# Kernel optimization log

Hardware: AMD Instinct MI355X
Metric: run time of the kernel (lower is better)

Reference implementation:

```python
import jax, jax.numpy as jnp
import numpy as np

B, H, S, D = 2, 12, 2048, 64

def setup_inputs() -> dict:
    key = jax.random.key(0)
    kq, kk, kv = jax.random.split(key, 3)
    Q = jax.random.normal(kq, (B, H, S, D), dtype=jnp.float32)
    K = jax.random.normal(kk, (B, H, S, D), dtype=jnp.float32)
    V = jax.random.normal(kv, (B, H, S, D), dtype=jnp.float32)
    return {"Q": Q, "K": K, "V": V}

def reference(Q, K, V):
    # NOTE: original code scales by sqrt(Q.shape[-2]) (the sequence length),
    # not the head dim — reproduced faithfully.
    scale = 1.0 / np.sqrt(Q.shape[-2]).astype(np.float32)
    scores = jnp.einsum('bhqd,bhkd->bhqk', Q, K) * scale  # [B,H,S,S]
    attn = jax.nn.softmax(scores, axis=-1)
    context = jnp.einsum('bhqk,bhkd->bhqd', attn, V)      # [B,H,S,D]
    # torch .squeeze(-1) only removes the last dim if it is size 1; D=64 so no-op
    return context
```

## Files before the change

kernel.cpp:

```cpp
#include <hip/hip_runtime.h>
#include <hip/hip_bf16.h>
#include <math.h>
#include <stdint.h>

#define BATCH 2
#define NH 12
#define SEQ 2048
#define HD 64
#define TQ 64
#define TK 64
#define NHEADS (BATCH*NH)
#define NIT (SEQ / TK)

typedef short bf16x8 __attribute__((ext_vector_type(8)));
typedef float f32x4 __attribute__((ext_vector_type(4)));
typedef float f32x16 __attribute__((ext_vector_type(16)));
typedef unsigned short us4_t __attribute__((ext_vector_type(4)));
typedef unsigned short us8_t __attribute__((ext_vector_type(8)));
typedef unsigned int u32x4 __attribute__((ext_vector_type(4)));

#if __has_builtin(__builtin_amdgcn_exp2f)
#define EXP2F(x) __builtin_amdgcn_exp2f(x)
#else
#define EXP2F(x) exp2f(x)
#endif

static __device__ __forceinline__ unsigned short f2bf(float f) {
    unsigned int u = __float_as_uint(f);
    u += 0x7fffu + ((u >> 16) & 1u);
    return (unsigned short)(u >> 16);
}

static __device__ __forceinline__ unsigned int pack2bf(float a, float b) {
    __hip_bfloat162 v = __float22bfloat162_rn(float2{a, b});
    return *(unsigned int*)&v;
}

static __device__ __forceinline__ void async_cp16(const void* g, void* l) {
    __builtin_amdgcn_global_load_lds(
        (const __attribute__((address_space(1))) void*)g,
        (__attribute__((address_space(3))) void*)(uintptr_t)l,
        16, 0, 0);
}

static __device__ __forceinline__ int tile_off(int r, int c) {
    int rp  = r >> 1;
    int pos = (((r & 1) << 3) | c) ^ (rp & 15);
    return rp * 128 + pos * 8;
}

__global__ __launch_bounds__(256)
void prep_kv(const float* __restrict__ K, const float* __restrict__ V,
             unsigned short* __restrict__ Kb, unsigned short* __restrict__ Vtb) {
    __shared__ unsigned short T[64][66];
    const int bh = blockIdx.x >> 5;
    const int s0 = (blockIdx.x & 31) * 64;
    const int tid = threadIdx.x;
    const size_t off = ((size_t)bh * SEQ + s0) * HD;

    #pragma unroll
    for (int u = 0; u < 4; ++u) {
        int idx = u * 1024 + tid * 4;
        float4 a = *(const float4*)&K[off + idx];
        us4_t r4 = { f2bf(a.x), f2bf(a.y), f2bf(a.z), f2bf(a.w) };
        *(us4_t*)&Kb[off + idx] = r4;
    }
    #pragma unroll
    for (int u = 0; u < 4; ++u) {
        int idx = u * 1024 + tid * 4;
        int r = idx >> 6, col = idx & 63;
        float4 a = *(const float4*)&V[off + idx];
        *(unsigned int*)&T[r][col]     = pack2bf(a.x, a.y);
        *(unsigned int*)&T[r][col + 2] = pack2bf(a.z, a.w);
    }
    __syncthreads();
    unsigned short* Vdst = Vtb + (size_t)bh * HD * SEQ;
    const int g = tid & 7, dd = tid >> 3;
    #pragma unroll
    for (int h = 0; h < 2; ++h) {
        int d = dd + 32 * h;
        us8_t r8;
        #pragma unroll
        for (int j = 0; j < 8; ++j) {
            int src = ((g >> 1) << 4) + ((j >> 2) << 3) + ((g & 1) << 2) + (j & 3);
            r8[j] = T[src][d];
        }
        *(us8_t*)&Vdst[(size_t)d * SEQ + s0 + g * 8] = r8;
    }
}

__global__ __launch_bounds__(256, 3)
void fa_main(const float* __restrict__ Q,
             const unsigned short* __restrict__ Kb,
             const unsigned short* __restrict__ Vtb,
             float* __restrict__ O, float qs) {
    const int x  = blockIdx.x & 7;
    const int t  = blockIdx.x >> 3;
    const int bh = x + 8 * (t % 3);
    const int qt = t / 3;
    const int q0 = qt * TQ;

    __shared__ __align__(16) unsigned char SH[33280];
    unsigned short* Ksh0 = (unsigned short*)SH;
    unsigned short* Ksh1 = (unsigned short*)(SH + 8192);
    unsigned short* Vsh0 = (unsigned short*)(SH + 16384);
    unsigned short* Vsh1 = (unsigned short*)(SH + 24576);
    float* Lsum = (float*)(SH + 32768);
    float* Linv = (float*)(SH + 33024);
    float* ORed = (float*)SH;

    const int tid  = threadIdx.x;
    const int w    = tid >> 6;
    const int mt   = w >> 1;
    const int nt   = w & 1;
    const int lane = tid & 63;
    const int l31  = lane & 31;
    const int hi   = lane >> 5;

    const float*          Qh = Q   + ((size_t)bh * SEQ + q0) * HD;
    const unsigned short* Kh = Kb  + (size_t)bh * SEQ * HD;
    const unsigned short* Vh = Vtb + (size_t)bh * HD * SEQ;

    int rS[2], cS[2];
    #pragma unroll
    for (int i = 0; i < 2; ++i) {
        int rp = w * 8 + 4 * i + (lane >> 4);
        int lc = (lane & 15) ^ (rp & 15);
        rS[i] = 2 * rp + (lc >> 3);
        cS[i] = lc & 7;
    }
    const int dst0 = (w * 8 + 0) * 128, dst1 = (w * 8 + 4) * 128;
    const size_t kG0 = (size_t)rS[0] * HD  + cS[0] * 8;
    const size_t kG1 = (size_t)rS[1] * HD  + cS[1] * 8;
    const size_t vG0 = (size_t)rS[0] * SEQ + cS[0] * 8;
    const size_t vG1 = (size_t)rS[1] * SEQ + cS[1] * 8;

    async_cp16(Kh + kG0, &Ksh0[dst0]);
    async_cp16(Kh + kG1, &Ksh0[dst1]);
    async_cp16(Vh + vG0, &Vsh0[dst0]);
    async_cp16(Vh + vG1, &Vsh0[dst1]);
    #pragma unroll
    for (int u = 0; u < 4; ++u) {
        int idx = u * 1024 + tid * 4;
        int r = idx >> 6, col = idx & 63;
        float4 a = *(const float4*)&Qh[idx];
        uint2 pk = { pack2bf(a.x * qs, a.y * qs), pack2bf(a.z * qs, a.w * qs) };
        *(uint2*)&Vsh1[tile_off(r, col >> 3) + (col & 7)] = pk;
    }
    __syncthreads();

    bf16x8 qf[4];
    #pragma unroll
    for (int s = 0; s < 4; ++s)
        qf[s] = *(const bf16x8*)&Vsh1[tile_off(mt * 32 + l31, s * 2 + hi)];
    __syncthreads();

    int kOffL[4], vOffL[2][2];
    #pragma unroll
    for (int s = 0; s < 4; ++s) kOffL[s] = tile_off(nt * 32 + l31, s * 2 + hi);
    #pragma unroll
    for (int dt = 0; dt < 2; ++dt)
        #pragma unroll
        for (int ks = 0; ks < 2; ++ks)
            vOffL[dt][ks] = tile_off(dt * 32 + l31, nt * 4 + ks * 2 + hi);

    f32x16 o[2];
    o[0] = (f32x16)(0.f);
    o[1] = (f32x16)(0.f);
    float lsum = 0.f;

    #pragma unroll 2
    for (int it = 0; it < NIT; ++it) {
        const int cur = it & 1;
        if (it + 1 < NIT) {
            const size_t kv = (size_t)(it + 1) * TK;
            unsigned short* Kn = cur ? Ksh0 : Ksh1;
            unsigned short* Vn = cur ? Vsh0 : Vsh1;
            async_cp16(Kh + kv * HD + kG0, &Kn[dst0]);
            async_cp16(Kh + kv * HD + kG1, &Kn[dst1]);
            async_cp16(Vh + kv + vG0,      &Vn[dst0]);
            async_cp16(Vh + kv + vG1,      &Vn[dst1]);
        }
        const unsigned short* Ks = cur ? Ksh1 : Ksh0;
        const unsigned short* Vs = cur ? Vsh1 : Vsh0;

        bf16x8 vf[2][2];
        #pragma unroll
        for (int dt = 0; dt < 2; ++dt)
            #pragma unroll
            for (int ks = 0; ks < 2; ++ks)
                vf[dt][ks] = *(const bf16x8*)&Vs[vOffL[dt][ks]];

        f32x16 sc = (f32x16)(0.f);
        __builtin_amdgcn_s_setprio(1);
        #pragma unroll
        for (int s = 0; s < 4; ++s) {
            bf16x8 kf = *(const bf16x8*)&Ks[kOffL[s]];
            sc = __builtin_amdgcn_mfma_f32_32x32x16_bf16(kf, qf[s], sc, 0, 0, 0);
        }
        __builtin_amdgcn_s_setprio(0);

        float e0[8], e1[8];
        #pragma unroll
        for (int r = 0; r < 8; ++r) e0[r] = EXP2F(sc[r]);
        union { u32x4 d; bf16x8 h; } pu0, pu1;
        pu0.d = (u32x4){ pack2bf(e0[0], e0[1]), pack2bf(e0[2], e0[3]),
                         pack2bf(e0[4], e0[5]), pack2bf(e0[6], e0[7]) };
        bf16x8 pf0 = pu0.h;
        __builtin_amdgcn_s_setprio(1);
        o[0] = __builtin_amdgcn_mfma_f32_32x32x16_bf16(pf0, vf[0][0], o[0], 0, 0, 0);
        o[1] = __builtin_amdgcn_mfma_f32_32x32x16_bf16(pf0, vf[1][0], o[1], 0, 0, 0);
        __builtin_amdgcn_s_setprio(0);

        #pragma unroll
        for (int r = 0; r < 8; ++r) e1[r] = EXP2F(sc[8 + r]);
        pu1.d = (u32x4){ pack2bf(e1[0], e1[1]), pack2bf(e1[2], e1[3]),
                         pack2bf(e1[4], e1[5]), pack2bf(e1[6], e1[7]) };
        bf16x8 pf1 = pu1.h;
        __builtin_amdgcn_s_setprio(1);
        o[0] = __builtin_amdgcn_mfma_f32_32x32x16_bf16(pf1, vf[0][1], o[0], 0, 0, 0);
        o[1] = __builtin_amdgcn_mfma_f32_32x32x16_bf16(pf1, vf[1][1], o[1], 0, 0, 0);
        __builtin_amdgcn_s_setprio(0);

        float t0 = ((e0[0] + e0[1]) + (e0[2] + e0[3]))
                 + ((e0[4] + e0[5]) + (e0[6] + e0[7]));
        float t1 = ((e1[0] + e1[1]) + (e1[2] + e1[3]))
                 + ((e1[4] + e1[5]) + (e1[6] + e1[7]));
        lsum += t0 + t1;

        __syncthreads();
    }

    lsum += __shfl_xor(lsum, 32, 64);

    if (nt == 1) {
        if (lane < 32) Lsum[mt * 32 + lane] = lsum;
        #pragma unroll
        for (int dt = 0; dt < 2; ++dt) {
            const int d = dt * 32 + l31;
            #pragma unroll
            for (int g = 0; g < 4; ++g) {
                const int m0 = mt * 32 + 8 * g + 4 * hi;
                const int ph = (m0 >> 2) ^ (d & 15);
                float4 v = { o[dt][4*g+0], o[dt][4*g+1], o[dt][4*g+2], o[dt][4*g+3] };
                *(float4*)&ORed[d * 64 + ph * 4] = v;
            }
        }
    }
    __syncthreads();

    if (nt == 0) {
        float ltot = lsum + Lsum[mt * 32 + l31];
        if (lane < 32) Linv[mt * 32 + lane] = 1.0f / ltot;
        float* Oh = O + ((size_t)bh * SEQ + q0) * HD;
        #pragma unroll
        for (int dt = 0; dt < 2; ++dt) {
            const int d = dt * 32 + l31;
            #pragma unroll
            for (int g = 0; g < 4; ++g) {
                const int m0 = mt * 32 + 8 * g + 4 * hi;
                const int ph = (m0 >> 2) ^ (d & 15);
                float4 part = *(const float4*)&ORed[d * 64 + ph * 4];
                float4 inv4 = *(const float4*)&Linv[m0];
                const float* pp = (const float*)&part;
                const float* ii = (const float*)&inv4;
                #pragma unroll
                for (int j = 0; j < 4; ++j)
                    Oh[(size_t)(m0 + j) * HD + d] = (o[dt][4*g+j] + pp[j]) * ii[j];
            }
        }
    }
}

#define PAD 8
#define LSTR (HD + PAD)

__global__ __launch_bounds__(256)
void fa_fwd_fb(const float* __restrict__ Q, const float* __restrict__ K,
               const float* __restrict__ V, float* __restrict__ O) {
    const int x  = blockIdx.x & 7;
    const int t  = blockIdx.x >> 3;
    const int bh = x + 8 * (t % 3);
    const int qt = t / 3;
    const int q0 = qt * TQ;
    const long base = (long)bh * SEQ * HD;

    __shared__ unsigned short Qs[TQ][LSTR];
    __shared__ unsigned short Ks2[64][LSTR];
    __shared__ unsigned short Vt[HD][64 + PAD];
    __shared__ unsigned short Ps2[4][16][LSTR];

    const int tid  = threadIdx.x;
    const int wave = tid >> 6;
    const int lane = tid & 63;
    const int col  = lane & 15;
    const int quad = lane >> 4;
    const int m0   = wave * 16;

    #pragma unroll
    for (int i = 0; i < 4; ++i) {
        int idx = tid + 256 * i;
        int row = idx >> 4;
        int c4  = (idx & 15) * 4;
        float4 v = *(const float4*)&Q[base + (long)(q0 + row) * HD + c4];
        ushort4 b = { f2bf(v.x), f2bf(v.y), f2bf(v.z), f2bf(v.w) };
        *(ushort4*)&Qs[row][c4] = b;
    }
    __syncthreads();

    bf16x8 aq0 = *(const bf16x8*)&Qs[m0 + col][quad * 8];
    bf16x8 aq1 = *(const bf16x8*)&Qs[m0 + col][32 + quad * 8];

    f32x4 o0 = {0.f,0.f,0.f,0.f}, o1 = o0, o2 = o0, o3 = o0;
    float l[4] = {0.f, 0.f, 0.f, 0.f};
    const float scale = 0.022097086912079608f;

    for (int kv0 = 0; kv0 < SEQ; kv0 += 64) {
        __syncthreads();
        #pragma unroll
        for (int i = 0; i < 4; ++i) {
            int idx = tid + 256 * i;
            int row = idx >> 4;
            int c4  = (idx & 15) * 4;
            float4 kv = *(const float4*)&K[base + (long)(kv0 + row) * HD + c4];
            ushort4 kb = { f2bf(kv.x), f2bf(kv.y), f2bf(kv.z), f2bf(kv.w) };
            *(ushort4*)&Ks2[row][c4] = kb;
            float4 vv = *(const float4*)&V[base + (long)(kv0 + row) * HD + c4];
            Vt[c4 + 0][row] = f2bf(vv.x);
            Vt[c4 + 1][row] = f2bf(vv.y);
            Vt[c4 + 2][row] = f2bf(vv.z);
            Vt[c4 + 3][row] = f2bf(vv.w);
        }
        __syncthreads();

        f32x4 sc[4];
        #pragma unroll
        for (int n = 0; n < 4; ++n) {
            bf16x8 b0 = *(const bf16x8*)&Ks2[n * 16 + col][quad * 8];
            bf16x8 b1 = *(const bf16x8*)&Ks2[n * 16 + col][32 + quad * 8];
            f32x4 acc = {0.f,0.f,0.f,0.f};
            acc = __builtin_amdgcn_mfma_f32_16x16x32_bf16(aq0, b0, acc, 0, 0, 0);
            acc = __builtin_amdgcn_mfma_f32_16x16x32_bf16(aq1, b1, acc, 0, 0, 0);
            sc[n] = acc;
        }

        float tsum[4] = {0.f, 0.f, 0.f, 0.f};
        #pragma unroll
        for (int n = 0; n < 4; ++n) {
            #pragma unroll
            for (int r = 0; r < 4; ++r) {
                float p = __expf(sc[n][r] * scale);
                tsum[r] += p;
                Ps2[wave][quad * 4 + r][n * 16 + col] = f2bf(p);
            }
        }
        #pragma unroll
        for (int off = 1; off < 16; off <<= 1) {
            #pragma unroll
            for (int r = 0; r < 4; ++r) tsum[r] += __shfl_xor(tsum[r], off, 64);
        }
        #pragma unroll
        for (int r = 0; r < 4; ++r) l[r] += tsum[r];

        bf16x8 ap0 = *(const bf16x8*)&Ps2[wave][col][quad * 8];
        bf16x8 ap1 = *(const bf16x8*)&Ps2[wave][col][32 + quad * 8];
        #pragma unroll
        for (int n = 0; n < 4; ++n) {
            bf16x8 b0 = *(const bf16x8*)&Vt[n * 16 + col][quad * 8];
            bf16x8 b1 = *(const bf16x8*)&Vt[n * 16 + col][32 + quad * 8];
            f32x4* op = (n == 0) ? &o0 : (n == 1) ? &o1 : (n == 2) ? &o2 : &o3;
            *op = __builtin_amdgcn_mfma_f32_16x16x32_bf16(ap0, b0, *op, 0, 0, 0);
            *op = __builtin_amdgcn_mfma_f32_16x16x32_bf16(ap1, b1, *op, 0, 0, 0);
        }
    }

    float inv[4];
    #pragma unroll
    for (int r = 0; r < 4; ++r) inv[r] = 1.0f / l[r];
    #pragma unroll
    for (int r = 0; r < 4; ++r) {
        long row = base + (long)(q0 + m0 + quad * 4 + r) * HD;
        O[row +  0 + col] = o0[r] * inv[r];
        O[row + 16 + col] = o1[r] * inv[r];
        O[row + 32 + col] = o2[r] * inv[r];
        O[row + 48 + col] = o3[r] * inv[r];
    }
}

extern "C" void kernel_launch(void* const* d_in, const int* in_sizes, int n_in,
                              void* d_out, int out_size, void* d_ws, size_t ws_size,
                              hipStream_t stream) {
    const float* Q = (const float*)d_in[0];
    const float* K = (const float*)d_in[1];
    const float* V = (const float*)d_in[2];
    float* O = (float*)d_out;

    const size_t tensorElems = (size_t)NHEADS * SEQ * HD;
    const size_t need = 2 * tensorElems * sizeof(unsigned short);

    if (ws_size >= need) {
        unsigned short* Kb  = (unsigned short*)d_ws;
        unsigned short* Vtb = Kb + tensorElems;
        const float qs = (float)(1.4426950408889634 / sqrt(2048.0));
        prep_kv<<<dim3(NHEADS * (SEQ / 64)), dim3(256), 0, stream>>>(K, V, Kb, Vtb);
        fa_main<<<dim3(NHEADS * (SEQ / TQ)), dim3(256), 0, stream>>>(Q, Kb, Vtb, O, qs);
    } else {
        fa_fwd_fb<<<dim3(NHEADS * (SEQ / TQ)), dim3(256), 0, stream>>>(Q, K, V, O);
    }
}
```

Measured before the change: 116.7 us.

## Triple-buffer K/V tiles with prefetch distance two and explicit vmcnt waits

Replaces the double-buffered K/V shared-memory pipeline with a three-stage ring buffer. The Q staging moves to its own region, and tiles are prefetched two iterations ahead. The end-of-loop __syncthreads is replaced by an s_waitcnt vmcnt plus s_barrier at the top of the loop, so up to two tiles of loads can be in flight while compute runs. Shared memory grows from about 33KB to about 49KB per block, which may lower occupancy under the 3-blocks-per-CU launch bound.

```diff
diff --git a/kernel.cpp b/kernel.cpp
--- a/kernel.cpp
+++ b/kernel.cpp
@@ -100,14 +100,11 @@
     const int qt = t / 3;
     const int q0 = qt * TQ;
 
-    __shared__ __align__(16) unsigned char SH[33280];
-    unsigned short* Ksh0 = (unsigned short*)SH;
-    unsigned short* Ksh1 = (unsigned short*)(SH + 8192);
-    unsigned short* Vsh0 = (unsigned short*)(SH + 16384);
-    unsigned short* Vsh1 = (unsigned short*)(SH + 24576);
-    float* Lsum = (float*)(SH + 32768);
-    float* Linv = (float*)(SH + 33024);
+    __shared__ __align__(16) unsigned char SH[49664];
+    float* Lsum = (float*)(SH + 49152);
+    float* Linv = (float*)(SH + 49408);
     float* ORed = (float*)SH;
+    unsigned short* QS = (unsigned short*)(SH + 32768);
 
     const int tid  = threadIdx.x;
     const int w    = tid >> 6;
@@ -135,25 +132,38 @@
     const size_t vG0 = (size_t)rS[0] * SEQ + cS[0] * 8;
     const size_t vG1 = (size_t)rS[1] * SEQ + cS[1] * 8;
 
-    async_cp16(Kh + kG0, &Ksh0[dst0]);
-    async_cp16(Kh + kG1, &Ksh0[dst1]);
-    async_cp16(Vh + vG0, &Vsh0[dst0]);
-    async_cp16(Vh + vG1, &Vsh0[dst1]);
+    {
+        unsigned short* K0 = (unsigned short*)(SH);
+        unsigned short* V0 = (unsigned short*)(SH + 8192);
+        async_cp16(Kh + kG0, &K0[dst0]);
+        async_cp16(Kh + kG1, &K0[dst1]);
+        async_cp16(Vh + vG0, &V0[dst0]);
+        async_cp16(Vh + vG1, &V0[dst1]);
+    }
     #pragma unroll
     for (int u = 0; u < 4; ++u) {
         int idx = u * 1024 + tid * 4;
         int r = idx >> 6, col = idx & 63;
         float4 a = *(const float4*)&Qh[idx];
         uint2 pk = { pack2bf(a.x * qs, a.y * qs), pack2bf(a.z * qs, a.w * qs) };
-        *(uint2*)&Vsh1[tile_off(r, col >> 3) + (col & 7)] = pk;
+        *(uint2*)&QS[tile_off(r, col >> 3) + (col & 7)] = pk;
     }
     __syncthreads();
 
     bf16x8 qf[4];
     #pragma unroll
     for (int s = 0; s < 4; ++s)
-        qf[s] = *(const bf16x8*)&Vsh1[tile_off(mt * 32 + l31, s * 2 + hi)];
+        qf[s] = *(const bf16x8*)&QS[tile_off(mt * 32 + l31, s * 2 + hi)];
     __syncthreads();
+
+    {
+        unsigned short* K1 = (unsigned short*)(SH + 16384);
+        unsigned short* V1 = (unsigned short*)(SH + 16384 + 8192);
+        async_cp16(Kh + (size_t)TK * HD + kG0, &K1[dst0]);
+        async_cp16(Kh + (size_t)TK * HD + kG1, &K1[dst1]);
+        async_cp16(Vh + (size_t)TK + vG0,      &V1[dst0]);
+        async_cp16(Vh + (size_t)TK + vG1,      &V1[dst1]);
+    }
 
     int kOffL[4], vOffL[2][2];
     #pragma unroll
@@ -169,20 +179,25 @@
     o[1] = (f32x16)(0.f);
     float lsum = 0.f;
 
+    unsigned int b0 = 0, b1 = 16384, b2 = 32768;
+
     #pragma unroll 2
     for (int it = 0; it < NIT; ++it) {
-        const int cur = it & 1;
-        if (it + 1 < NIT) {
-            const size_t kv = (size_t)(it + 1) * TK;
-            unsigned short* Kn = cur ? Ksh0 : Ksh1;
-            unsigned short* Vn = cur ? Vsh0 : Vsh1;
+        if (it == NIT - 1) { asm volatile("s_waitcnt vmcnt(0)" ::: "memory"); }
+        else               { asm volatile("s_waitcnt vmcnt(4)" ::: "memory"); }
+        __builtin_amdgcn_s_barrier();
+
+        if (it + 2 < NIT) {
+            const size_t kv = (size_t)(it + 2) * TK;
+            unsigned short* Kn = (unsigned short*)(SH + b2);
+            unsigned short* Vn = (unsigned short*)(SH + b2 + 8192);
             async_cp16(Kh + kv * HD + kG0, &Kn[dst0]);
             async_cp16(Kh + kv * HD + kG1, &Kn[dst1]);
             async_cp16(Vh + kv + vG0,      &Vn[dst0]);
             async_cp16(Vh + kv + vG1,      &Vn[dst1]);
         }
-        const unsigned short* Ks = cur ? Ksh1 : Ksh0;
-        const unsigned short* Vs = cur ? Vsh1 : Vsh0;
+        const unsigned short* Ks = (const unsigned short*)(SH + b0);
+        const unsigned short* Vs = (const unsigned short*)(SH + b0 + 8192);
 
         bf16x8 vf[2][2];
         #pragma unroll
@@ -228,7 +243,7 @@
                  + ((e1[4] + e1[5]) + (e1[6] + e1[7]));
         lsum += t0 + t1;
 
-        __syncthreads();
+        unsigned int btmp = b0; b0 = b1; b1 = b2; b2 = btmp;
     }
 
     lsum += __shfl_xor(lsum, 32, 64);
```

After: 117.5 us. Within noise of the previous version (+0.6%).

## Load K/V fragments directly from global into registers, dropping LDS staging

Applied to the files above, without the earlier changes.

Replaces the double-buffered async global-to-LDS staging of K and V tiles with direct per-lane global loads of the MFMA fragments into registers, prefetched one iteration ahead. This removes the per-iteration __syncthreads and the LDS reads, and shrinks shared memory. In exchange each wave now fetches its own fragments straight from global/L2 (waves sharing nt load the same K data, so reuse moves from LDS to cache). The extra prefetch registers may also lower occupancy.

```diff
diff --git a/kernel.cpp b/kernel.cpp
--- a/kernel.cpp
+++ b/kernel.cpp
@@ -34,13 +34,6 @@
 static __device__ __forceinline__ unsigned int pack2bf(float a, float b) {
     __hip_bfloat162 v = __float22bfloat162_rn(float2{a, b});
     return *(unsigned int*)&v;
-}
-
-static __device__ __forceinline__ void async_cp16(const void* g, void* l) {
-    __builtin_amdgcn_global_load_lds(
-        (const __attribute__((address_space(1))) void*)g,
-        (__attribute__((address_space(3))) void*)(uintptr_t)l,
-        16, 0, 0);
 }
 
 static __device__ __forceinline__ int tile_off(int r, int c) {
@@ -100,14 +93,11 @@
     const int qt = t / 3;
     const int q0 = qt * TQ;
 
-    __shared__ __align__(16) unsigned char SH[33280];
-    unsigned short* Ksh0 = (unsigned short*)SH;
-    unsigned short* Ksh1 = (unsigned short*)(SH + 8192);
-    unsigned short* Vsh0 = (unsigned short*)(SH + 16384);
-    unsigned short* Vsh1 = (unsigned short*)(SH + 24576);
-    float* Lsum = (float*)(SH + 32768);
-    float* Linv = (float*)(SH + 33024);
+    __shared__ __align__(16) unsigned char SH[16896];
+    unsigned short* QS = (unsigned short*)SH;
     float* ORed = (float*)SH;
+    float* Lsum = (float*)(SH + 16384);
+    float* Linv = (float*)(SH + 16640);
 
     const int tid  = threadIdx.x;
     const int w    = tid >> 6;
@@ -121,48 +111,35 @@
     const unsigned short* Kh = Kb  + (size_t)bh * SEQ * HD;
     const unsigned short* Vh = Vtb + (size_t)bh * HD * SEQ;
 
-    int rS[2], cS[2];
-    #pragma unroll
-    for (int i = 0; i < 2; ++i) {
-        int rp = w * 8 + 4 * i + (lane >> 4);
-        int lc = (lane & 15) ^ (rp & 15);
-        rS[i] = 2 * rp + (lc >> 3);
-        cS[i] = lc & 7;
-    }
-    const int dst0 = (w * 8 + 0) * 128, dst1 = (w * 8 + 4) * 128;
-    const size_t kG0 = (size_t)rS[0] * HD  + cS[0] * 8;
-    const size_t kG1 = (size_t)rS[1] * HD  + cS[1] * 8;
-    const size_t vG0 = (size_t)rS[0] * SEQ + cS[0] * 8;
-    const size_t vG1 = (size_t)rS[1] * SEQ + cS[1] * 8;
-
-    async_cp16(Kh + kG0, &Ksh0[dst0]);
-    async_cp16(Kh + kG1, &Ksh0[dst1]);
-    async_cp16(Vh + vG0, &Vsh0[dst0]);
-    async_cp16(Vh + vG1, &Vsh0[dst1]);
     #pragma unroll
     for (int u = 0; u < 4; ++u) {
         int idx = u * 1024 + tid * 4;
         int r = idx >> 6, col = idx & 63;
         float4 a = *(const float4*)&Qh[idx];
         uint2 pk = { pack2bf(a.x * qs, a.y * qs), pack2bf(a.z * qs, a.w * qs) };
-        *(uint2*)&Vsh1[tile_off(r, col >> 3) + (col & 7)] = pk;
-    }
-    __syncthreads();
-
+        *(uint2*)&QS[tile_off(r, col >> 3) + (col & 7)] = pk;
+    }
+    __syncthreads();
     bf16x8 qf[4];
     #pragma unroll
     for (int s = 0; s < 4; ++s)
-        qf[s] = *(const bf16x8*)&Vsh1[tile_off(mt * 32 + l31, s * 2 + hi)];
-    __syncthreads();
-
-    int kOffL[4], vOffL[2][2];
-    #pragma unroll
-    for (int s = 0; s < 4; ++s) kOffL[s] = tile_off(nt * 32 + l31, s * 2 + hi);
-    #pragma unroll
-    for (int dt = 0; dt < 2; ++dt)
-        #pragma unroll
-        for (int ks = 0; ks < 2; ++ks)
-            vOffL[dt][ks] = tile_off(dt * 32 + l31, nt * 4 + ks * 2 + hi);
+        qf[s] = *(const bf16x8*)&QS[tile_off(mt * 32 + l31, s * 2 + hi)];
+    __syncthreads();
+
+    const unsigned short* kP  = Kh + (size_t)(nt * 32 + l31) * HD + hi * 8;
+    const unsigned short* vP0 = Vh + (size_t)(l31) * SEQ        + (nt * 4 + hi) * 8;
+    const unsigned short* vP1 = Vh + (size_t)(32 + l31) * SEQ   + (nt * 4 + hi) * 8;
+
+    bf16x8 kc[4], vc[2][2], kn[4], vn[2][2];
+    #pragma unroll
+    for (int s = 0; s < 4; ++s) kc[s] = *(const bf16x8*)(kP + s * 16);
+    vc[0][0] = *(const bf16x8*)(vP0);
+    vc[0][1] = *(const bf16x8*)(vP0 + 16);
+    vc[1][0] = *(const bf16x8*)(vP1);
+    vc[1][1] = *(const bf16x8*)(vP1 + 16);
+    const unsigned short* kPn  = kP  + (size_t)TK * HD;
+    const unsigned short* vP0n = vP0 + TK;
+    const unsigned short* vP1n = vP1 + TK;
 
     f32x16 o[2];
     o[0] = (f32x16)(0.f);
@@ -171,33 +148,23 @@
 
     #pragma unroll 2
     for (int it = 0; it < NIT; ++it) {
-        const int cur = it & 1;
         if (it + 1 < NIT) {
-            const size_t kv = (size_t)(it + 1) * TK;
-            unsigned short* Kn = cur ? Ksh0 : Ksh1;
-            unsigned short* Vn = cur ? Vsh0 : Vsh1;
-            async_cp16(Kh + kv * HD + kG0, &Kn[dst0]);
-            async_cp16(Kh + kv * HD + kG1, &Kn[dst1]);
-            async_cp16(Vh + kv + vG0,      &Vn[dst0]);
-            async_cp16(Vh + kv + vG1,      &Vn[dst1]);
-        }
-        const unsigned short* Ks = cur ? Ksh1 : Ksh0;
-        const unsigned short* Vs = cur ? Vsh1 : Vsh0;
-
-        bf16x8 vf[2][2];
-        #pragma unroll
-        for (int dt = 0; dt < 2; ++dt)
-            #pragma unroll
-            for (int ks = 0; ks < 2; ++ks)
-                vf[dt][ks] = *(const bf16x8*)&Vs[vOffL[dt][ks]];
+            #pragma unroll
+            for (int s = 0; s < 4; ++s) kn[s] = *(const bf16x8*)(kPn + s * 16);
+            vn[0][0] = *(const bf16x8*)(vP0n);
+            vn[0][1] = *(const bf16x8*)(vP0n + 16);
+            vn[1][0] = *(const bf16x8*)(vP1n);
+            vn[1][1] = *(const bf16x8*)(vP1n + 16);
+            kPn  += (size_t)TK * HD;
+            vP0n += TK;
+            vP1n += TK;
+        }
 
         f32x16 sc = (f32x16)(0.f);
         __builtin_amdgcn_s_setprio(1);
         #pragma unroll
-        for (int s = 0; s < 4; ++s) {
-            bf16x8 kf = *(const bf16x8*)&Ks[kOffL[s]];
-            sc = __builtin_amdgcn_mfma_f32_32x32x16_bf16(kf, qf[s], sc, 0, 0, 0);
-        }
+        for (int s = 0; s < 4; ++s)
+            sc = __builtin_amdgcn_mfma_f32_32x32x16_bf16(kc[s], qf[s], sc, 0, 0, 0);
         __builtin_amdgcn_s_setprio(0);
 
         float e0[8], e1[8];
@@ -208,8 +175,8 @@
                          pack2bf(e0[4], e0[5]), pack2bf(e0[6], e0[7]) };
         bf16x8 pf0 = pu0.h;
         __builtin_amdgcn_s_setprio(1);
-        o[0] = __builtin_amdgcn_mfma_f32_32x32x16_bf16(pf0, vf[0][0], o[0], 0, 0, 0);
-        o[1] = __builtin_amdgcn_mfma_f32_32x32x16_bf16(pf0, vf[1][0], o[1], 0, 0, 0);
+        o[0] = __builtin_amdgcn_mfma_f32_32x32x16_bf16(pf0, vc[0][0], o[0], 0, 0, 0);
+        o[1] = __builtin_amdgcn_mfma_f32_32x32x16_bf16(pf0, vc[1][0], o[1], 0, 0, 0);
         __builtin_amdgcn_s_setprio(0);
 
         #pragma unroll
@@ -218,8 +185,8 @@
                          pack2bf(e1[4], e1[5]), pack2bf(e1[6], e1[7]) };
         bf16x8 pf1 = pu1.h;
         __builtin_amdgcn_s_setprio(1);
-        o[0] = __builtin_amdgcn_mfma_f32_32x32x16_bf16(pf1, vf[0][1], o[0], 0, 0, 0);
-        o[1] = __builtin_amdgcn_mfma_f32_32x32x16_bf16(pf1, vf[1][1], o[1], 0, 0, 0);
+        o[0] = __builtin_amdgcn_mfma_f32_32x32x16_bf16(pf1, vc[0][1], o[0], 0, 0, 0);
+        o[1] = __builtin_amdgcn_mfma_f32_32x32x16_bf16(pf1, vc[1][1], o[1], 0, 0, 0);
         __builtin_amdgcn_s_setprio(0);
 
         float t0 = ((e0[0] + e0[1]) + (e0[2] + e0[3]))
@@ -228,7 +195,13 @@
                  + ((e1[4] + e1[5]) + (e1[6] + e1[7]));
         lsum += t0 + t1;
 
-        __syncthreads();
+        #pragma unroll
+        for (int s = 0; s < 4; ++s) kc[s] = kn[s];
+        #pragma unroll
+        for (int dt = 0; dt < 2; ++dt)
+            #pragma unroll
+            for (int ks = 0; ks < 2; ++ks)
+                vc[dt][ks] = vn[dt][ks];
     }
 
     lsum += __shfl_xor(lsum, 32, 64);
```

New measurement: 168.7 us. 44.5% more time.
